# Performance work log

Measured on AMD Instinct MI355X. Metric: run time of the kernel, lower is better.

## Reference

```python
import jax, jax.numpy as jnp
import numpy as np

C_REG = 0.1
MAX_ITER = 15
FEAT_SCALE = 0.05  # keep linear-kernel entries O(1) for a well-conditioned QP


def batched_kronecker(a, b):
    # a: (B,n,m), b: (B,p,q) -> (B, n*p, m*q); matches torch batched_kronecker
    B, n, m = a.shape
    _, p, q = b.shape
    return jnp.einsum('bij,bkl->bikjl', a, b).reshape(B, n * p, m * q)


def solve_qp_batch(G, e, h, A, b, max_iter):
    # Solves min_z 0.5 z^T G z + e^T z  s.t.  z <= h (C = I), A z = b
    # via a primal-dual interior-point method, batched over tasks.
    # (Same QP as qpth.QPFunction with C = identity.)
    def solve_one(G, e, h, A, b):
        nz = G.shape[0]
        neq = A.shape[0]
        nineq = h.shape[0]  # == nz since C = I
        z0 = jnp.zeros(nz, G.dtype)
        nu0 = jnp.zeros(neq, G.dtype)
        s0 = jnp.ones(nineq, G.dtype)
        lam0 = jnp.ones(nineq, G.dtype)

        def step(carry, _):
            z, nu, s, lam = carry
            rd = G @ z + e + lam + A.T @ nu          # dual residual (C^T lam = lam)
            rp = z + s - h                            # primal ineq residual (C z = z)
            rp2 = A @ z - b                           # primal eq residual
            mu = jnp.dot(s, lam) / nineq
            rc = lam * s - 0.1 * mu                   # centered complementarity
            d = lam / s
            H = G + jnp.diag(d)                       # G + C^T diag(lam/s) C with C = I
            r1 = -rd + (rc - lam * rp) / s
            KKT = jnp.block([[H, A.T], [A, jnp.zeros((neq, neq), G.dtype)]])
            rhs = jnp.concatenate([r1, -rp2])
            sol = jnp.linalg.solve(KKT, rhs)
            dz = sol[:nz]
            dnu = sol[nz:]
            ds = -rp - dz
            dlam = (-rc - lam * ds) / s
            a_s = jnp.min(jnp.where(ds < 0, -s / ds, jnp.inf))
            a_l = jnp.min(jnp.where(dlam < 0, -lam / dlam, jnp.inf))
            alpha = jnp.minimum(1.0, 0.99 * jnp.minimum(a_s, a_l))
            return (z + alpha * dz, nu + alpha * dnu, s + alpha * ds, lam + alpha * dlam), None

        (z, _, _, _), _ = jax.lax.scan(step, (z0, nu0, s0, lam0), None, length=max_iter)
        return z

    return jax.vmap(solve_one)(G, e, h, A, b)


def setup_inputs() -> dict:
    key = jax.random.key(0)
    k1, k2, k3 = jax.random.split(key, 3)
    B, N, K, Q, D = 32, 10, 10, 15, 512
    support = jax.random.normal(k1, (B, N, K, D), dtype=jnp.float32) * FEAT_SCALE
    support_labels = jax.random.randint(k2, (B, N, K), 0, N)
    query = jax.random.normal(k3, (B, N, Q, D), dtype=jnp.float32) * FEAT_SCALE
    return {"support": support, "support_labels": support_labels, "query": query}


def reference(support, support_labels, query):
    B, N, K, D = support.shape
    Q = query.shape[2]
    n_way = N
    n_support = N * K
    sup = support.reshape(B, n_support, D)
    qry = query.reshape(B, N * Q, D)

    # Gram matrix and block-kronecker QP Hessian: G = K(sup,sup) kron I_nway + I
    kernel = jnp.einsum('bnd,bmd->bnm', sup, sup)
    I_way = jnp.broadcast_to(jnp.eye(n_way, dtype=sup.dtype), (B, n_way, n_way))
    G = batched_kronecker(kernel, I_way) + jnp.eye(n_way * n_support, dtype=sup.dtype)

    y = jax.nn.one_hot(support_labels.reshape(B, n_support), n_way, dtype=sup.dtype)
    y_flat = y.reshape(B, n_support * n_way)
    e = -y_flat
    h = C_REG * y_flat

    # A = I_nsupport kron ones(1, n_way): sums alphas over classes per support point
    I_sup = jnp.broadcast_to(jnp.eye(n_support, dtype=sup.dtype), (B, n_support, n_support))
    A = batched_kronecker(I_sup, jnp.ones((B, 1, n_way), dtype=sup.dtype))
    b = jnp.zeros((B, n_support), dtype=sup.dtype)

    qp_sol = solve_qp_batch(G, e, h, A, b, MAX_ITER)  # (B, n_support*n_way)

    compat = jnp.einsum('bnd,bmd->bnm', sup, qry)     # (B, n_support, n_query)
    qp_sol = qp_sol.reshape(B, n_support, n_way)
    logits = jnp.einsum('bsq,bsn->bqn', compat, qp_sol)  # (B, n_query, n_way)
    return logits
```

## Files before the change

### kernel.cpp

```cpp
#include <hip/hip_runtime.h>

constexpr int kB   = 32;
constexpr int kNS  = 100;
constexpr int kNW  = 10;
constexpr int kNZ  = 1000;
constexpr int kD   = 512;
constexpr int kNQ  = 150;
constexpr int kIt  = 15;
constexpr int kPan = 4;
constexpr int kGrp = 8;
constexpr int kRQ  = 13;
constexpr int kNSP = kGrp * kRQ;

__global__ __launch_bounds__(256) void gemm_kernel(const float* __restrict__ sup,
                                                   const float* __restrict__ qry,
                                                   float* __restrict__ Kf,
                                                   float* __restrict__ compat)
{
    const int i0 = blockIdx.x * 2;
    const int b  = blockIdx.y;
    const int w    = threadIdx.x >> 6;
    const int lane = threadIdx.x & 63;
    const float* supb = sup + (size_t)b * kNS * kD;
    const float* qryb = qry + (size_t)b * kNQ * kD;
    const float4* r0 = reinterpret_cast<const float4*>(supb + (size_t)i0 * kD) + 2 * lane;
    const float4* r1 = reinterpret_cast<const float4*>(supb + (size_t)(i0 + 1) * kD) + 2 * lane;
    const float4 a0 = r0[0], a1 = r0[1];
    const float4 q0 = r1[0], q1 = r1[1];
    for (int t = w; t < kNS + kNQ; t += 4) {
        const float* rowt = (t < kNS) ? (supb + (size_t)t * kD)
                                      : (qryb + (size_t)(t - kNS) * kD);
        const float4* rt = reinterpret_cast<const float4*>(rowt) + 2 * lane;
        const float4 v0 = rt[0], v1 = rt[1];
        float pa = a0.x*v0.x + a0.y*v0.y + a0.z*v0.z + a0.w*v0.w
                 + a1.x*v1.x + a1.y*v1.y + a1.z*v1.z + a1.w*v1.w;
        float pb = q0.x*v0.x + q0.y*v0.y + q0.z*v0.z + q0.w*v0.w
                 + q1.x*v1.x + q1.y*v1.y + q1.z*v1.z + q1.w*v1.w;
        #pragma unroll
        for (int msk = 1; msk < 64; msk <<= 1) {
            pa += __shfl_xor(pa, msk);
            pb += __shfl_xor(pb, msk);
        }
        if (lane == 0) {
            if (t < kNS) {
                Kf[((size_t)b * kNS + i0    ) * kNS + t] = pa;
                Kf[((size_t)b * kNS + i0 + 1) * kNS + t] = pb;
            } else {
                compat[((size_t)b * kNS + i0    ) * kNQ + (t - kNS)] = pa;
                compat[((size_t)b * kNS + i0 + 1) * kNQ + (t - kNS)] = pb;
            }
        }
    }
}

__global__ __launch_bounds__(256) void init_kernel(double* __restrict__ z,
                                                   double* __restrict__ nu,
                                                   double* __restrict__ s,
                                                   double* __restrict__ lam,
                                                   double* __restrict__ mu_g,
                                                   float* __restrict__ Sg)
{
    const int b = blockIdx.x;
    const int tid = threadIdx.x;
    for (int m = tid; m < kNZ; m += 256) {
        z[b*kNZ + m]   = 0.0;
        s[b*kNZ + m]   = 1.0;
        lam[b*kNZ + m] = 1.0;
    }
    for (int e = tid; e < kNS * kNS; e += 256) Sg[(size_t)b * kNS * kNS + e] = 0.0f;
    if (tid < kNS) nu[b*kNS + tid] = 0.0;
    if (tid == 0)  mu_g[b] = 1.0;
}

__device__ __forceinline__ void adj4_solvef(const float B[4][4],
                                            const float b1[4], const float b2[4],
                                            float m1[4], float m2[4])
{
    const float s0 = B[0][0]*B[1][1] - B[1][0]*B[0][1];
    const float s1 = B[0][0]*B[1][2] - B[1][0]*B[0][2];
    const float s2 = B[0][0]*B[1][3] - B[1][0]*B[0][3];
    const float s3 = B[0][1]*B[1][2] - B[1][1]*B[0][2];
    const float s4 = B[0][1]*B[1][3] - B[1][1]*B[0][3];
    const float s5 = B[0][2]*B[1][3] - B[1][2]*B[0][3];
    const float c5 = B[2][2]*B[3][3] - B[3][2]*B[2][3];
    const float c4 = B[2][1]*B[3][3] - B[3][1]*B[2][3];
    const float c3 = B[2][1]*B[3][2] - B[3][1]*B[2][2];
    const float c2 = B[2][0]*B[3][3] - B[3][0]*B[2][3];
    const float c1 = B[2][0]*B[3][2] - B[3][0]*B[2][2];
    const float c0 = B[2][0]*B[3][1] - B[3][0]*B[2][1];
    const float det = s0*c5 - s1*c4 + s2*c3 + s3*c2 - s4*c1 + s5*c0;
    const float id = 1.0f / det;
    {
        const float r0 = ( B[1][1]*c5 - B[1][2]*c4 + B[1][3]*c3) * id;
        const float r1 = (-B[0][1]*c5 + B[0][2]*c4 - B[0][3]*c3) * id;
        const float r2 = ( B[3][1]*s5 - B[3][2]*s4 + B[3][3]*s3) * id;
        const float r3 = (-B[2][1]*s5 + B[2][2]*s4 - B[2][3]*s3) * id;
        m1[0] = r0*b1[0] + r1*b1[1] + r2*b1[2] + r3*b1[3];
        m2[0] = r0*b2[0] + r1*b2[1] + r2*b2[2] + r3*b2[3];
    }
    {
        const float r0 = (-B[1][0]*c5 + B[1][2]*c2 - B[1][3]*c1) * id;
        const float r1 = ( B[0][0]*c5 - B[0][2]*c2 + B[0][3]*c1) * id;
        const float r2 = (-B[3][0]*s5 + B[3][2]*s2 - B[3][3]*s1) * id;
        const float r3 = ( B[2][0]*s5 - B[2][2]*s2 + B[2][3]*s1) * id;
        m1[1] = r0*b1[0] + r1*b1[1] + r2*b1[2] + r3*b1[3];
        m2[1] = r0*b2[0] + r1*b2[1] + r2*b2[2] + r3*b2[3];
    }
    {
        const float r0 = ( B[1][0]*c4 - B[1][1]*c2 + B[1][3]*c0) * id;
        const float r1 = (-B[0][0]*c4 + B[0][1]*c2 - B[0][3]*c0) * id;
        const float r2 = ( B[3][0]*s4 - B[3][1]*s2 + B[3][3]*s0) * id;
        const float r3 = (-B[2][0]*s4 + B[2][1]*s2 - B[2][3]*s0) * id;
        m1[2] = r0*b1[0] + r1*b1[1] + r2*b1[2] + r3*b1[3];
        m2[2] = r0*b2[0] + r1*b2[1] + r2*b2[2] + r3*b2[3];
    }
    {
        const float r0 = (-B[1][0]*c3 + B[1][1]*c1 - B[1][2]*c0) * id;
        const float r1 = ( B[0][0]*c3 - B[0][1]*c1 + B[0][2]*c0) * id;
        const float r2 = (-B[3][0]*s3 + B[3][1]*s1 - B[3][2]*s0) * id;
        const float r3 = ( B[2][0]*s3 - B[2][1]*s1 + B[2][2]*s0) * id;
        m1[3] = r0*b1[0] + r1*b1[1] + r2*b1[2] + r3*b1[3];
        m2[3] = r0*b2[0] + r1*b2[1] + r2*b2[2] + r3*b2[3];
    }
}

#define PANEL_UPDATE2F(H1, H2, WSG, BUF, BASE, SCL1, SCL2, M1, M2)            \
    {                                                                          \
        _Pragma("unroll")                                                      \
        for (int r = 0; r < kRQ; ++r) { H1[r] *= SCL1; H2[r] *= SCL2; }        \
        _Pragma("unroll")                                                      \
        for (int p = 0; p < kPan; ++p) {                                       \
            const float mp1 = M1[p], mp2 = M2[p];                              \
            float w[kRQ];                                                      \
            _Pragma("unroll")                                                  \
            for (int u = 0; u < kRQ; ++u) w[u] = WSG[BUF][p][BASE + u];        \
            __builtin_amdgcn_sched_barrier(0);                                 \
            _Pragma("unroll")                                                  \
            for (int u = 0; u < kRQ; ++u) {                                    \
                H1[u] = fmaf(-mp1, w[u], H1[u]);                               \
                H2[u] = fmaf(-mp2, w[u], H2[u]);                               \
            }                                                                  \
        }                                                                      \
    }

__global__ __launch_bounds__(512) void ipm_invert_kernel(
    const float* __restrict__ Kf, const int* __restrict__ labels,
    double* __restrict__ z, double* __restrict__ s, double* __restrict__ lam,
    const double* __restrict__ nu_in, double* __restrict__ nu_out,
    const double* __restrict__ dnu_g, const double* __restrict__ dz_g,
    const double* __restrict__ ds_g, const double* __restrict__ dl_g,
    const double* __restrict__ minr_g, const double* __restrict__ part3_g,
    double* __restrict__ mu_g,
    float* __restrict__ Hinv, float* __restrict__ Sg,
    double* __restrict__ tvec, const int first)
{
    const int b = blockIdx.x / kNW;
    const int a = blockIdx.x - b * kNW;
    const int tid = threadIdx.x;
    const int h = tid >> 6;
    const int lane = tid & 63;
    const int base = h * kRQ;
    const int j1 = lane;
    const int j2 = 64 + lane;
    const bool a2 = (j2 < kNS);
    const int js2 = a2 ? j2 : j1;

    __shared__ double za[kNS], sa[kNS], la[kNS], nus[kNS], r1s[kNS];
    __shared__ float  daf[kNS];
    __shared__ double part[kGrp][kNS];
    __shared__ alignas(16) float Wr [2][kPan][kNSP + 8];
    __shared__ alignas(16) float Wsg[2][kPan][kNSP + 8];
    __shared__ int labs[kNS];

    const float* Kb = Kf + (size_t)b * kNS * kNS;

    double mu = 1.0;
    if (tid < kNS) {
        double alpha = 0.0;
        if (!first) {
            double am = 1e300;
            #pragma unroll
            for (int aa = 0; aa < kNW; ++aa) am = fmin(am, minr_g[b * kNW + aa]);
            alpha = fmin(1.0, 0.99 * am);
            double P0 = 0.0, P1 = 0.0, P2 = 0.0;
            #pragma unroll
            for (int aa = 0; aa < kNW; ++aa) {
                const double* pp = part3_g + (size_t)(b * kNW + aa) * 3;
                P0 += pp[0]; P1 += pp[1]; P2 += pp[2];
            }
            mu = (P0 + alpha * (P1 + alpha * P2)) / kNZ;
        }
        const size_t m = (size_t)b * kNZ + tid * kNW + a;
        double zv = z[m], sv = s[m], lv = lam[m];
        double nv = nu_in[b * kNS + tid];
        if (!first) {
            zv += alpha * dz_g[m]; sv += alpha * ds_g[m]; lv += alpha * dl_g[m];
            z[m] = zv; s[m] = sv; lam[m] = lv;
            nv += alpha * dnu_g[b * kNS + tid];
        }
        if (a == 0) {
            nu_out[b * kNS + tid] = nv;
            if (tid == 0) mu_g[b] = mu;
        }
        za[tid] = zv; sa[tid] = sv; la[tid] = lv;
        daf[tid] = (float)(lv / sv);
        nus[tid] = nv;
        labs[tid] = labels[b * kNS + tid];
    }
    if (h == 0 && j2 >= kNS && j2 < kNSP) {
        #pragma unroll
        for (int bf = 0; bf < 2; ++bf)
            #pragma unroll
            for (int p = 0; p < kPan; ++p) { Wr[bf][p][j2] = 0.0f; Wsg[bf][p][j2] = 0.0f; }
    }
    __syncthreads();

    float h1[kRQ], h2[kRQ];
    double kz1 = 0.0, kz2 = 0.0;
    #pragma unroll
    for (int r = 0; r < kRQ; ++r) {
        const int i = base + r;
        if (i < kNS) {
            float kv1 = Kb[(size_t)i * kNS + j1];
            float kv2 = Kb[(size_t)i * kNS + js2];
            kz1 += (double)kv1 * za[i];
            kz2 += (double)kv2 * za[i];
            h1[r] = (i == j1)  ? (kv1 + 1.0f + daf[j1])  : kv1;
            h2[r] = (i == js2) ? (kv2 + 1.0f + daf[js2]) : kv2;
        } else { h1[r] = 0.0f; h2[r] = 0.0f; }
    }
    part[h][j1] = kz1;
    if (a2) part[h][j2] = kz2;
    if (h == 0) {
        #pragma unroll
        for (int p = 0; p < kPan; ++p) {
            Wr [0][p][j1] = h1[p];  Wsg[0][p][j1] = h1[p];
            if (a2) { Wr[0][p][j2] = h2[p]; Wsg[0][p][j2] = h2[p]; }
        }
    }
    __syncthreads();
    if (tid < kNS) {
        const int i = tid;
        double kz = 0.0;
        #pragma unroll
        for (int g = 0; g < kGrp; ++g) kz += part[g][i];
        double yv = (labs[i] == a) ? 1.0 : 0.0;
        double rd = kz + za[i] - yv + la[i] + nus[i];
        double rp = za[i] + sa[i] - 0.1 * yv;
        double rc = la[i] * sa[i] - 0.1 * mu;
        r1s[i] = -rd + (rc - la[i] * rp) / sa[i];
    }

    #pragma unroll 1
    for (int k0 = 0; k0 < kNS; k0 += kPan) {
        const int buf = (k0 >> 2) & 1, nbuf = 1 - buf;
        __syncthreads();
        float B[4][4];
        #pragma unroll
        for (int p = 0; p < 4; ++p)
            #pragma unroll
            for (int q = 0; q < 4; ++q)
                B[p][q] = Wr[buf][p][k0 + q];

        const bool inp1 = (j1 >= k0) && (j1 < k0 + kPan);
        const bool inp2 = (js2 >= k0) && (js2 < k0 + kPan);
        float b1[4], b2[4];
        #pragma unroll
        for (int p = 0; p < 4; ++p) {
            b1[p] = inp1 ? ((j1  - k0 == p) ? 1.0f : 0.0f) : Wr[buf][p][j1];
            b2[p] = inp2 ? ((js2 - k0 == p) ? 1.0f : 0.0f) : Wr[buf][p][js2];
        }
        float m1[4], m2[4];
        adj4_solvef(B, b1, b2, m1, m2);
        const float scl1 = inp1 ? 0.0f : 1.0f;
        const float scl2 = inp2 ? 0.0f : 1.0f;
        PANEL_UPDATE2F(h1, h2, Wsg, buf, base, scl1, scl2, m1, m2);

        if (k0 < base + kRQ && k0 + kPan - 1 >= base) {
            #pragma unroll
            for (int r = 0; r < kRQ; ++r) {
                const int i = base + r;
                if (i >= k0 && i < k0 + kPan) {
                    const int p = i - k0;
                    h1[r] = m1[p];
                    h2[r] = m2[p];
                }
            }
        }
        const int kn0 = k0 + kPan;
        if (kn0 < kNS && kn0 < base + kRQ && kn0 + kPan - 1 >= base) {
            #pragma unroll
            for (int r = 0; r < kRQ; ++r) {
                const int i = base + r;
                if (i >= kn0 && i < kn0 + kPan) {
                    const int p = i - kn0;
                    Wr [nbuf][p][j1] = h1[r];
                    Wsg[nbuf][p][j1] = (j1 < kn0) ? -h1[r] : h1[r];
                    if (a2) {
                        Wr [nbuf][p][j2] = h2[r];
                        Wsg[nbuf][p][j2] = (j2 < kn0) ? -h2[r] : h2[r];
                    }
                }
            }
        }
    }

    float* Hb = Hinv + (size_t)(b * kNW + a) * kNS * kNS;
    float* Sb = Sg   + (size_t)b * kNS * kNS;
    double tp1 = 0.0, tp2 = 0.0;
    #pragma unroll
    for (int r = 0; r < kRQ; ++r) {
        const int i = base + r;
        if (i < kNS) {
            Hb[(size_t)i * kNS + j1] = h1[r];
            atomicAdd(&Sb[(size_t)i * kNS + j1], h1[r]);
            tp1 += (double)h1[r] * r1s[i];
            if (a2) {
                Hb[(size_t)i * kNS + j2] = h2[r];
                atomicAdd(&Sb[(size_t)i * kNS + j2], h2[r]);
                tp2 += (double)h2[r] * r1s[i];
            }
        }
    }
    part[h][j1] = tp1;
    if (a2) part[h][j2] = tp2;
    __syncthreads();
    if (tid < kNS) {
        double t = 0.0;
        #pragma unroll
        for (int g = 0; g < kGrp; ++g) t += part[g][tid];
        tvec[(size_t)(b * kNW + a) * kNS + tid] = t;
    }
}

__global__ __launch_bounds__(512) void schur_solve_kernel(
    const float* __restrict__ Sg, const double* __restrict__ tvec,
    const double* __restrict__ z, double* __restrict__ dnu_g)
{
    const int b = blockIdx.x;
    const int tid = threadIdx.x;
    const int h = tid >> 6;
    const int lane = tid & 63;
    const int base = h * kRQ;
    const int j1 = lane;
    const int j2 = 64 + lane;
    const bool a2 = (j2 <= kNS);
    const int js2 = a2 ? j2 : j1;

    __shared__ double rhs[kNS];
    __shared__ alignas(16) float Wr [2][kPan][kNSP + 8];
    __shared__ alignas(16) float Wsg[2][kPan][kNSP + 8];

    const float*  Sb = Sg   + (size_t)b * kNS * kNS;
    const double* tb = tvec + (size_t)b * kNW * kNS;
    const double* zb = z    + (size_t)b * kNZ;

    if (tid < kNS) {
        double acc = 0.0, rp2 = 0.0;
        #pragma unroll
        for (int a = 0; a < kNW; ++a) {
            acc += tb[a * kNS + tid];
            rp2 += zb[tid * kNW + a];
        }
        rhs[tid] = acc + rp2;
    }
    if (h == 0 && j2 > kNS && j2 < kNSP) {
        #pragma unroll
        for (int bf = 0; bf < 2; ++bf)
            #pragma unroll
            for (int p = 0; p < kPan; ++p) { Wr[bf][p][j2] = 0.0f; Wsg[bf][p][j2] = 0.0f; }
    }
    __syncthreads();

    float h1[kRQ], h2[kRQ];
    #pragma unroll
    for (int r = 0; r < kRQ; ++r) {
        const int i = base + r;
        if (i < kNS) {
            h1[r] = Sb[(size_t)i * kNS + j1];
            h2[r] = (js2 == kNS) ? (float)rhs[i]
                  : Sb[(size_t)i * kNS + ((js2 < kNS) ? js2 : 0)];
        } else { h1[r] = 0.0f; h2[r] = 0.0f; }
    }
    if (h == 0) {
        #pragma unroll
        for (int p = 0; p < kPan; ++p) {
            Wr [0][p][j1] = h1[p];  Wsg[0][p][j1] = h1[p];
            if (a2) { Wr[0][p][j2] = h2[p]; Wsg[0][p][j2] = h2[p]; }
        }
    }

    #pragma unroll 1
    for (int k0 = 0; k0 < kNS; k0 += kPan) {
        const int buf = (k0 >> 2) & 1, nbuf = 1 - buf;
        __syncthreads();
        float B[4][4];
        #pragma unroll
        for (int p = 0; p < 4; ++p)
            #pragma unroll
            for (int q = 0; q < 4; ++q)
                B[p][q] = Wr[buf][p][k0 + q];

        const bool inp1 = (j1 >= k0) && (j1 < k0 + kPan);
        const bool inp2 = (js2 >= k0) && (js2 < k0 + kPan);
        float b1[4], b2[4];
        #pragma unroll
        for (int p = 0; p < 4; ++p) {
            b1[p] = inp1 ? ((j1  - k0 == p) ? 1.0f : 0.0f) : Wr[buf][p][j1];
            b2[p] = inp2 ? ((js2 - k0 == p) ? 1.0f : 0.0f) : Wr[buf][p][js2];
        }
        float m1[4], m2[4];
        adj4_solvef(B, b1, b2, m1, m2);
        const float scl1 = inp1 ? 0.0f : 1.0f;
        const float scl2 = inp2 ? 0.0f : 1.0f;
        PANEL_UPDATE2F(h1, h2, Wsg, buf, base, scl1, scl2, m1, m2);

        if (k0 < base + kRQ && k0 + kPan - 1 >= base) {
            #pragma unroll
            for (int r = 0; r < kRQ; ++r) {
                const int i = base + r;
                if (i >= k0 && i < k0 + kPan) {
                    const int p = i - k0;
                    h1[r] = m1[p];
                    h2[r] = m2[p];
                }
            }
        }
        const int kn0 = k0 + kPan;
        if (kn0 < kNS && kn0 < base + kRQ && kn0 + kPan - 1 >= base) {
            #pragma unroll
            for (int r = 0; r < kRQ; ++r) {
                const int i = base + r;
                if (i >= kn0 && i < kn0 + kPan) {
                    const int p = i - kn0;
                    Wr [nbuf][p][j1] = h1[r];
                    Wsg[nbuf][p][j1] = (j1 < kn0) ? -h1[r] : h1[r];
                    if (a2) {
                        Wr [nbuf][p][j2] = h2[r];
                        Wsg[nbuf][p][j2] = (j2 < kn0) ? -h2[r] : h2[r];
                    }
                }
            }
        }
    }

    if (j2 == kNS) {
        #pragma unroll
        for (int r = 0; r < kRQ; ++r) {
            const int i = base + r;
            if (i < kNS) dnu_g[(size_t)b * kNS + i] = (double)h2[r];
        }
    }
}

__global__ __launch_bounds__(512) void dz_kernel(
    const int* __restrict__ labels,
    const float* __restrict__ Hinv, const double* __restrict__ tvec,
    const double* __restrict__ dnu_g,
    const double* __restrict__ z, const double* __restrict__ s,
    const double* __restrict__ lam, const double* __restrict__ mu_g,
    double* __restrict__ dz_g, double* __restrict__ ds_g,
    double* __restrict__ dl_g, double* __restrict__ minr_g,
    double* __restrict__ part3_g, float* __restrict__ Sg)
{
    const int b = blockIdx.x / kNW;
    const int a = blockIdx.x - b * kNW;
    const int tid = threadIdx.x;
    const int h = tid >> 7;
    const int j = tid & 127;

    __shared__ double dnus[kNS];
    __shared__ double p4[4][kNS];
    __shared__ double red[512], rA[512], rB[512], rC[512];

    const float* Hb = Hinv + (size_t)(b * kNW + a) * kNS * kNS;

    if (tid < kNS) dnus[tid] = dnu_g[(size_t)b * kNS + tid];
    {
        float* Sb = Sg + (size_t)b * kNS * kNS + (size_t)a * (kNS * kNS / kNW);
        for (int e = tid; e < kNS * kNS / kNW; e += 512) Sb[e] = 0.0f;
    }
    __syncthreads();

    if (j < kNS) {
        double p = 0.0;
        #pragma unroll
        for (int r = 0; r < kNS / 4; ++r)
            p += (double)Hb[(size_t)(h * (kNS / 4) + r) * kNS + j] * dnus[h * (kNS / 4) + r];
        p4[h][j] = p;
    }
    __syncthreads();

    double lmin = 1e300, p0 = 0.0, p1 = 0.0, p2 = 0.0;
    if (tid < kNS) {
        const int i = tid;
        const size_t m = (size_t)b * kNZ + i * kNW + a;
        const double mu = mu_g[b];
        double dz = tvec[(size_t)(b * kNW + a) * kNS + i]
                  - (p4[0][i] + p4[1][i] + p4[2][i] + p4[3][i]);
        double yv = (labels[b * kNS + i] == a) ? 1.0 : 0.0;
        double zv = z[m], sv = s[m], lv = lam[m];
        double rp = zv + sv - 0.1 * yv;
        double rc = lv * sv - 0.1 * mu;
        double ds = -rp - dz;
        double dl = (-rc - lv * ds) / sv;
        dz_g[m] = dz; ds_g[m] = ds; dl_g[m] = dl;
        if (ds < 0.0) lmin = fmin(lmin, -sv / ds);
        if (dl < 0.0) lmin = fmin(lmin, -lv / dl);
        p0 = sv * lv;
        p1 = sv * dl + lv * ds;
        p2 = ds * dl;
    }
    red[tid] = lmin; rA[tid] = p0; rB[tid] = p1; rC[tid] = p2;
    __syncthreads();
    for (int off = 256; off > 0; off >>= 1) {
        if (tid < off) {
            red[tid] = fmin(red[tid], red[tid + off]);
            rA[tid] += rA[tid + off];
            rB[tid] += rB[tid + off];
            rC[tid] += rC[tid + off];
        }
        __syncthreads();
    }
    if (tid == 0) {
        minr_g[b * kNW + a] = red[0];
        double* pp = part3_g + (size_t)(b * kNW + a) * 3;
        pp[0] = rA[0]; pp[1] = rB[0]; pp[2] = rC[0];
    }
}

__global__ __launch_bounds__(256) void logits_kernel(const float* __restrict__ compat,
                                                     const double* __restrict__ z,
                                                     const double* __restrict__ dz_g,
                                                     const double* __restrict__ minr_g,
                                                     float* __restrict__ out)
{
    const int b = blockIdx.x;
    const int tid = threadIdx.x;
    const float* cb = compat + (size_t)b * kNS * kNQ;
    const double* zb = z + (size_t)b * kNZ;
    __shared__ double zs[kNZ];
    double am = 1e300;
    #pragma unroll
    for (int aa = 0; aa < kNW; ++aa) am = fmin(am, minr_g[b * kNW + aa]);
    const double alpha = fmin(1.0, 0.99 * am);
    for (int m = tid; m < kNZ; m += 256)
        zs[m] = zb[m] + alpha * dz_g[(size_t)b * kNZ + m];
    __syncthreads();
    for (int idx = tid; idx < kNQ * kNW; idx += 256) {
        int q = idx / kNW, n = idx - q * kNW;
        double acc = 0.0;
        for (int s2 = 0; s2 < kNS; ++s2)
            acc += (double)cb[(size_t)s2 * kNQ + q] * zs[s2 * kNW + n];
        out[(size_t)b * kNQ * kNW + idx] = (float)acc;
    }
}

extern "C" void kernel_launch(void* const* d_in, const int* in_sizes, int n_in,
                              void* d_out, int out_size, void* d_ws, size_t ws_size,
                              hipStream_t stream)
{
    const float* sup    = (const float*)d_in[0];
    const int*   labels = (const int*)  d_in[1];
    const float* qry    = (const float*)d_in[2];
    float* out = (float*)d_out;

    char* ws = (char*)d_ws;
    size_t off = 0;
    auto alloc = [&](size_t bytes) -> void* {
        void* p = ws + off;
        off += (bytes + 255) & ~(size_t)255;
        return p;
    };
    float*  Kf     = (float*) alloc(sizeof(float)  * kB * kNS * kNS);
    double* z      = (double*)alloc(sizeof(double) * kB * kNZ);
    double* nuA    = (double*)alloc(sizeof(double) * kB * kNS);
    double* nuB    = (double*)alloc(sizeof(double) * kB * kNS);
    double* s      = (double*)alloc(sizeof(double) * kB * kNZ);
    double* lam    = (double*)alloc(sizeof(double) * kB * kNZ);
    double* mu_g   = (double*)alloc(sizeof(double) * kB);
    float*  Hinv   = (float*) alloc(sizeof(float)  * kB * kNW * kNS * kNS);
    float*  Sg     = (float*) alloc(sizeof(float)  * kB * kNS * kNS);
    double* tvec   = (double*)alloc(sizeof(double) * kB * kNW * kNS);
    double* dnu_g  = (double*)alloc(sizeof(double) * kB * kNS);
    double* dz_g   = (double*)alloc(sizeof(double) * kB * kNZ);
    double* ds_g   = (double*)alloc(sizeof(double) * kB * kNZ);
    double* dl_g   = (double*)alloc(sizeof(double) * kB * kNZ);
    double* minr_g = (double*)alloc(sizeof(double) * kB * kNW);
    double* part3_g= (double*)alloc(sizeof(double) * kB * kNW * 3);
    float*  compat = (float*) alloc(sizeof(float)  * kB * kNS * kNQ);

    gemm_kernel<<<dim3(kNS / 2, kB), 256, 0, stream>>>(sup, qry, Kf, compat);
    init_kernel<<<kB, 256, 0, stream>>>(z, nuA, s, lam, mu_g, Sg);

    for (int it = 0; it < kIt; ++it) {
        const double* nu_in  = (it & 1) ? nuB : nuA;
        double*       nu_out = (it & 1) ? nuA : nuB;
        ipm_invert_kernel<<<kB * kNW, 512, 0, stream>>>(
            Kf, labels, z, s, lam, nu_in, nu_out,
            dnu_g, dz_g, ds_g, dl_g, minr_g, part3_g, mu_g,
            Hinv, Sg, tvec, (it == 0) ? 1 : 0);
        schur_solve_kernel<<<kB, 512, 0, stream>>>(Sg, tvec, z, dnu_g);
        dz_kernel<<<kB * kNW, 512, 0, stream>>>(labels, Hinv, tvec, dnu_g,
                                                z, s, lam, mu_g,
                                                dz_g, ds_g, dl_g, minr_g,
                                                part3_g, Sg);
    }

    logits_kernel<<<kB, 256, 0, stream>>>(compat, z, dz_g, minr_g, out);
}
```

Baseline: 2.423 ms.

## Widen Gauss-Jordan panel to 8 with blocked 2x2 pivot solve; split logits grid

The panel width of the in-shared-memory Gauss-Jordan inversion and Schur solve grows from 4 to 8 columns. Each 8x8 pivot block is solved with a 4x4 adjugate inverse plus a 4x4 Schur complement. This halves the number of panel steps and __syncthreads barriers, at the cost of more per-thread arithmetic and register pressure. The RHS column is remapped to a padded slot, and identity padding is injected so the 100 rows tile cleanly into panels of 8. The logits kernel is also split across 10 blocks per batch for more parallelism.

```diff
diff --git a/kernel.cpp b/kernel.cpp
--- a/kernel.cpp
+++ b/kernel.cpp
@@ -7,7 +7,7 @@
 constexpr int kD   = 512;
 constexpr int kNQ  = 150;
 constexpr int kIt  = 15;
-constexpr int kPan = 4;
+constexpr int kPan = 8;
 constexpr int kGrp = 8;
 constexpr int kRQ  = 13;
 constexpr int kNSP = kGrp * kRQ;
@@ -70,6 +70,40 @@
     for (int e = tid; e < kNS * kNS; e += 256) Sg[(size_t)b * kNS * kNS + e] = 0.0f;
     if (tid < kNS) nu[b*kNS + tid] = 0.0;
     if (tid == 0)  mu_g[b] = 1.0;
+}
+
+__device__ __forceinline__ void adj4_invf(const float B[4][4], float I4[4][4])
+{
+    const float s0 = B[0][0]*B[1][1] - B[1][0]*B[0][1];
+    const float s1 = B[0][0]*B[1][2] - B[1][0]*B[0][2];
+    const float s2 = B[0][0]*B[1][3] - B[1][0]*B[0][3];
+    const float s3 = B[0][1]*B[1][2] - B[1][1]*B[0][2];
+    const float s4 = B[0][1]*B[1][3] - B[1][1]*B[0][3];
+    const float s5 = B[0][2]*B[1][3] - B[1][2]*B[0][3];
+    const float c5 = B[2][2]*B[3][3] - B[3][2]*B[2][3];
+    const float c4 = B[2][1]*B[3][3] - B[3][1]*B[2][3];
+    const float c3 = B[2][1]*B[3][2] - B[3][1]*B[2][2];
+    const float c2 = B[2][0]*B[3][3] - B[3][0]*B[2][3];
+    const float c1 = B[2][0]*B[3][2] - B[3][0]*B[2][2];
+    const float c0 = B[2][0]*B[3][1] - B[3][0]*B[2][1];
+    const float det = s0*c5 - s1*c4 + s2*c3 + s3*c2 - s4*c1 + s5*c0;
+    const float id = 1.0f / det;
+    I4[0][0] = ( B[1][1]*c5 - B[1][2]*c4 + B[1][3]*c3) * id;
+    I4[0][1] = (-B[0][1]*c5 + B[0][2]*c4 - B[0][3]*c3) * id;
+    I4[0][2] = ( B[3][1]*s5 - B[3][2]*s4 + B[3][3]*s3) * id;
+    I4[0][3] = (-B[2][1]*s5 + B[2][2]*s4 - B[2][3]*s3) * id;
+    I4[1][0] = (-B[1][0]*c5 + B[1][2]*c2 - B[1][3]*c1) * id;
+    I4[1][1] = ( B[0][0]*c5 - B[0][2]*c2 + B[0][3]*c1) * id;
+    I4[1][2] = (-B[3][0]*s5 + B[3][2]*s2 - B[3][3]*s1) * id;
+    I4[1][3] = ( B[2][0]*s5 - B[2][2]*s2 + B[2][3]*s1) * id;
+    I4[2][0] = ( B[1][0]*c4 - B[1][1]*c2 + B[1][3]*c0) * id;
+    I4[2][1] = (-B[0][0]*c4 + B[0][1]*c2 - B[0][3]*c0) * id;
+    I4[2][2] = ( B[3][0]*s4 - B[3][1]*s2 + B[3][3]*s0) * id;
+    I4[2][3] = (-B[2][0]*s4 + B[2][1]*s2 - B[2][3]*s0) * id;
+    I4[3][0] = (-B[1][0]*c3 + B[1][1]*c1 - B[1][2]*c0) * id;
+    I4[3][1] = ( B[0][0]*c3 - B[0][1]*c1 + B[0][2]*c0) * id;
+    I4[3][2] = (-B[3][0]*s3 + B[3][1]*s1 - B[3][2]*s0) * id;
+    I4[3][3] = ( B[2][0]*s3 - B[2][1]*s1 + B[2][2]*s0) * id;
 }
 
 __device__ __forceinline__ void adj4_solvef(const float B[4][4],
@@ -143,6 +177,84 @@
         }                                                                      \
     }
 
+#define PIVOT8_SOLVE(WR, BUF, K0, INP1, INP2, JC1, JC2, J1K, J2K, M1, M2)     \
+    float M1[kPan], M2[kPan];                                                  \
+    {                                                                          \
+        float Ainv[4][4], AiB[4][4], y1[4], y2[4];                             \
+        {                                                                      \
+            float A4[4][4];                                                    \
+            _Pragma("unroll")                                                  \
+            for (int p = 0; p < 4; ++p)                                        \
+                _Pragma("unroll")                                              \
+                for (int q = 0; q < 4; ++q) A4[p][q] = WR[BUF][p][K0 + q];     \
+            adj4_invf(A4, Ainv);                                               \
+        }                                                                      \
+        {                                                                      \
+            float Bm[4][4];                                                    \
+            _Pragma("unroll")                                                  \
+            for (int p = 0; p < 4; ++p)                                        \
+                _Pragma("unroll")                                              \
+                for (int q = 0; q < 4; ++q) Bm[p][q] = WR[BUF][p][K0 + 4 + q]; \
+            _Pragma("unroll")                                                  \
+            for (int p = 0; p < 4; ++p)                                        \
+                _Pragma("unroll")                                              \
+                for (int q = 0; q < 4; ++q)                                    \
+                    AiB[p][q] = Ainv[p][0]*Bm[0][q] + Ainv[p][1]*Bm[1][q]      \
+                              + Ainv[p][2]*Bm[2][q] + Ainv[p][3]*Bm[3][q];     \
+        }                                                                      \
+        {                                                                      \
+            float bl1[4], bl2[4];                                              \
+            _Pragma("unroll")                                                  \
+            for (int p = 0; p < 4; ++p) {                                      \
+                bl1[p] = INP1 ? ((J1K == p) ? 1.0f : 0.0f) : WR[BUF][p][JC1];  \
+                bl2[p] = INP2 ? ((J2K == p) ? 1.0f : 0.0f) : WR[BUF][p][JC2];  \
+            }                                                                  \
+            _Pragma("unroll")                                                  \
+            for (int p = 0; p < 4; ++p) {                                      \
+                y1[p] = Ainv[p][0]*bl1[0] + Ainv[p][1]*bl1[1]                  \
+                      + Ainv[p][2]*bl1[2] + Ainv[p][3]*bl1[3];                 \
+                y2[p] = Ainv[p][0]*bl2[0] + Ainv[p][1]*bl2[1]                  \
+                      + Ainv[p][2]*bl2[2] + Ainv[p][3]*bl2[3];                 \
+            }                                                                  \
+        }                                                                      \
+        {                                                                      \
+            float Cm[4][4], S4[4][4], t1[4], t2[4];                            \
+            _Pragma("unroll")                                                  \
+            for (int p = 0; p < 4; ++p)                                        \
+                _Pragma("unroll")                                              \
+                for (int q = 0; q < 4; ++q) Cm[p][q] = WR[BUF][4 + p][K0 + q]; \
+            _Pragma("unroll")                                                  \
+            for (int p = 0; p < 4; ++p)                                        \
+                _Pragma("unroll")                                              \
+                for (int q = 0; q < 4; ++q)                                    \
+                    S4[p][q] = WR[BUF][4 + p][K0 + 4 + q]                      \
+                             - (Cm[p][0]*AiB[0][q] + Cm[p][1]*AiB[1][q]        \
+                              + Cm[p][2]*AiB[2][q] + Cm[p][3]*AiB[3][q]);      \
+            _Pragma("unroll")                                                  \
+            for (int p = 0; p < 4; ++p) {                                      \
+                const float bh1 = INP1 ? ((J1K == 4 + p) ? 1.0f : 0.0f)        \
+                                       : WR[BUF][4 + p][JC1];                  \
+                const float bh2 = INP2 ? ((J2K == 4 + p) ? 1.0f : 0.0f)        \
+                                       : WR[BUF][4 + p][JC2];                  \
+                t1[p] = bh1 - (Cm[p][0]*y1[0] + Cm[p][1]*y1[1]                 \
+                             + Cm[p][2]*y1[2] + Cm[p][3]*y1[3]);               \
+                t2[p] = bh2 - (Cm[p][0]*y2[0] + Cm[p][1]*y2[1]                 \
+                             + Cm[p][2]*y2[2] + Cm[p][3]*y2[3]);               \
+            }                                                                  \
+            float xh1[4], xh2[4];                                              \
+            adj4_solvef(S4, t1, t2, xh1, xh2);                                 \
+            _Pragma("unroll")                                                  \
+            for (int p = 0; p < 4; ++p) {                                      \
+                M1[4 + p] = xh1[p];                                            \
+                M2[4 + p] = xh2[p];                                            \
+                M1[p] = y1[p] - (AiB[p][0]*xh1[0] + AiB[p][1]*xh1[1]           \
+                               + AiB[p][2]*xh1[2] + AiB[p][3]*xh1[3]);         \
+                M2[p] = y2[p] - (AiB[p][0]*xh2[0] + AiB[p][1]*xh2[1]           \
+                               + AiB[p][2]*xh2[2] + AiB[p][3]*xh2[3]);         \
+            }                                                                  \
+        }                                                                      \
+    }
+
 __global__ __launch_bounds__(512) void ipm_invert_kernel(
     const float* __restrict__ Kf, const int* __restrict__ labels,
     double* __restrict__ z, double* __restrict__ s, double* __restrict__ lam,
@@ -253,25 +365,14 @@
 
     #pragma unroll 1
     for (int k0 = 0; k0 < kNS; k0 += kPan) {
-        const int buf = (k0 >> 2) & 1, nbuf = 1 - buf;
+        const int buf = (k0 / kPan) & 1, nbuf = 1 - buf;
         __syncthreads();
-        float B[4][4];
-        #pragma unroll
-        for (int p = 0; p < 4; ++p)
-            #pragma unroll
-            for (int q = 0; q < 4; ++q)
-                B[p][q] = Wr[buf][p][k0 + q];
 
         const bool inp1 = (j1 >= k0) && (j1 < k0 + kPan);
         const bool inp2 = (js2 >= k0) && (js2 < k0 + kPan);
-        float b1[4], b2[4];
-        #pragma unroll
-        for (int p = 0; p < 4; ++p) {
-            b1[p] = inp1 ? ((j1  - k0 == p) ? 1.0f : 0.0f) : Wr[buf][p][j1];
-            b2[p] = inp2 ? ((js2 - k0 == p) ? 1.0f : 0.0f) : Wr[buf][p][js2];
-        }
-        float m1[4], m2[4];
-        adj4_solvef(B, b1, b2, m1, m2);
+        const int  j1k  = j1  - k0;
+        const int  j2k  = js2 - k0;
+        PIVOT8_SOLVE(Wr, buf, k0, inp1, inp2, j1, js2, j1k, j2k, m1, m2);
         const float scl1 = inp1 ? 0.0f : 1.0f;
         const float scl2 = inp2 ? 0.0f : 1.0f;
         PANEL_UPDATE2F(h1, h2, Wsg, buf, base, scl1, scl2, m1, m2);
@@ -303,6 +404,10 @@
                 }
             }
         }
+        if (kn0 == 96 && tid < 4) {
+            Wr [nbuf][4 + tid][100 + tid] = 1.0f;
+            Wsg[nbuf][4 + tid][100 + tid] = 1.0f;
+        }
     }
 
     float* Hb = Hinv + (size_t)(b * kNW + a) * kNS * kNS;
@@ -345,7 +450,9 @@
     const int j1 = lane;
     const int j2 = 64 + lane;
     const bool a2 = (j2 <= kNS);
+    const bool isrhs = (j2 == kNS);
     const int js2 = a2 ? j2 : j1;
+    const int jc2 = isrhs ? kNSP : js2;
 
     __shared__ double rhs[kNS];
     __shared__ alignas(16) float Wr [2][kPan][kNSP + 8];
@@ -364,7 +471,7 @@
         }
         rhs[tid] = acc + rp2;
     }
-    if (h == 0 && j2 > kNS && j2 < kNSP) {
+    if (h == 0 && j2 >= kNS && j2 < kNSP) {
         #pragma unroll
         for (int bf = 0; bf < 2; ++bf)
             #pragma unroll
@@ -378,7 +485,7 @@
         const int i = base + r;
         if (i < kNS) {
             h1[r] = Sb[(size_t)i * kNS + j1];
-            h2[r] = (js2 == kNS) ? (float)rhs[i]
+            h2[r] = isrhs ? (float)rhs[i]
                   : Sb[(size_t)i * kNS + ((js2 < kNS) ? js2 : 0)];
         } else { h1[r] = 0.0f; h2[r] = 0.0f; }
     }
@@ -386,31 +493,20 @@
         #pragma unroll
         for (int p = 0; p < kPan; ++p) {
             Wr [0][p][j1] = h1[p];  Wsg[0][p][j1] = h1[p];
-            if (a2) { Wr[0][p][j2] = h2[p]; Wsg[0][p][j2] = h2[p]; }
+            if (a2) { Wr[0][p][jc2] = h2[p]; Wsg[0][p][jc2] = h2[p]; }
         }
     }
 
     #pragma unroll 1
     for (int k0 = 0; k0 < kNS; k0 += kPan) {
-        const int buf = (k0 >> 2) & 1, nbuf = 1 - buf;
+        const int buf = (k0 / kPan) & 1, nbuf = 1 - buf;
         __syncthreads();
-        float B[4][4];
-        #pragma unroll
-        for (int p = 0; p < 4; ++p)
-            #pragma unroll
-            for (int q = 0; q < 4; ++q)
-                B[p][q] = Wr[buf][p][k0 + q];
 
         const bool inp1 = (j1 >= k0) && (j1 < k0 + kPan);
-        const bool inp2 = (js2 >= k0) && (js2 < k0 + kPan);
-        float b1[4], b2[4];
-        #pragma unroll
-        for (int p = 0; p < 4; ++p) {
-            b1[p] = inp1 ? ((j1  - k0 == p) ? 1.0f : 0.0f) : Wr[buf][p][j1];
-            b2[p] = inp2 ? ((js2 - k0 == p) ? 1.0f : 0.0f) : Wr[buf][p][js2];
-        }
-        float m1[4], m2[4];
-        adj4_solvef(B, b1, b2, m1, m2);
+        const bool inp2 = !isrhs && (js2 >= k0) && (js2 < k0 + kPan);
+        const int  j1k  = j1  - k0;
+        const int  j2k  = js2 - k0;
+        PIVOT8_SOLVE(Wr, buf, k0, inp1, inp2, j1, jc2, j1k, j2k, m1, m2);
         const float scl1 = inp1 ? 0.0f : 1.0f;
         const float scl2 = inp2 ? 0.0f : 1.0f;
         PANEL_UPDATE2F(h1, h2, Wsg, buf, base, scl1, scl2, m1, m2);
@@ -436,15 +532,19 @@
                     Wr [nbuf][p][j1] = h1[r];
                     Wsg[nbuf][p][j1] = (j1 < kn0) ? -h1[r] : h1[r];
                     if (a2) {
-                        Wr [nbuf][p][j2] = h2[r];
-                        Wsg[nbuf][p][j2] = (j2 < kn0) ? -h2[r] : h2[r];
+                        Wr [nbuf][p][jc2] = h2[r];
+                        Wsg[nbuf][p][jc2] = (j2 < kn0) ? -h2[r] : h2[r];
                     }
                 }
             }
         }
-    }
-
-    if (j2 == kNS) {
+        if (kn0 == 96 && tid < 4) {
+            Wr [nbuf][4 + tid][100 + tid] = 1.0f;
+            Wsg[nbuf][4 + tid][100 + tid] = 1.0f;
+        }
+    }
+
+    if (isrhs) {
         #pragma unroll
         for (int r = 0; r < kRQ; ++r) {
             const int i = base + r;
@@ -535,7 +635,8 @@
                                                      const double* __restrict__ minr_g,
                                                      float* __restrict__ out)
 {
-    const int b = blockIdx.x;
+    const int b = blockIdx.x / kNW;
+    const int c = blockIdx.x - b * kNW;
     const int tid = threadIdx.x;
     const float* cb = compat + (size_t)b * kNS * kNQ;
     const double* zb = z + (size_t)b * kNZ;
@@ -547,12 +648,13 @@
     for (int m = tid; m < kNZ; m += 256)
         zs[m] = zb[m] + alpha * dz_g[(size_t)b * kNZ + m];
     __syncthreads();
-    for (int idx = tid; idx < kNQ * kNW; idx += 256) {
-        int q = idx / kNW, n = idx - q * kNW;
+    for (int idx = tid; idx < (kNQ / kNW) * kNW; idx += 256) {
+        int ql = idx / kNW, n = idx - ql * kNW;
+        int q = c * (kNQ / kNW) + ql;
         double acc = 0.0;
         for (int s2 = 0; s2 < kNS; ++s2)
             acc += (double)cb[(size_t)s2 * kNQ + q] * zs[s2 * kNW + n];
-        out[(size_t)b * kNQ * kNW + idx] = (float)acc;
+        out[(size_t)b * kNQ * kNW + q * kNW + n] = (float)acc;
     }
 }
 
@@ -607,5 +709,5 @@
                                                 part3_g, Sg);
     }
 
-    logits_kernel<<<kB, 256, 0, stream>>>(compat, z, dz_g, minr_g, out);
-}
+    logits_kernel<<<kB * kNW, 256, 0, stream>>>(compat, z, dz_g, minr_g, out);
+}
```

New measurement: 3.137 ms. +29.5%, slower.
